# Optimization experiments

Hardware: AMD Instinct MI355X
Metric: run time of the kernel (lower is better)

Reference implementation:

```python
import jax, jax.numpy as jnp
import numpy as np


def setup_inputs() -> dict:
    key = jax.random.key(0)
    k1, k2, k3, k4 = jax.random.split(key, 4)
    B, Nq, Nk, D = 8, 2048, 2048, 768
    return {
        "query": jax.random.normal(k1, (B, Nq, D), dtype=jnp.float32),
        "key": jax.random.normal(k2, (Nk, D), dtype=jnp.float32),
        "x": jax.random.normal(k3, (B, Nk, D), dtype=jnp.float32),
        "W": jax.random.normal(k4, (D, D), dtype=jnp.float32) * (1.0 / np.sqrt(D)),
        "b": jnp.zeros((D,), dtype=jnp.float32),
    }


def reference(query, key, x, W, b):
    # Linear projection: [B,Nq,dk] @ W^T + b -> [B,Nq,dq]
    query_proj = jnp.einsum("bqd,ed->bqe", query, W) + b
    # tensordot over dim_query: [B,Nq,dq] x [Nk,dq] -> [B,Nq,Nk]
    score = jnp.einsum("bqe,ke->bqk", query_proj, key)
    attn = jax.nn.softmax(score, axis=-1)
    # bmm: [B,Nq,Nk] @ [B,Nk,Dv] -> [B,Nq,Dv]
    out = jnp.einsum("bqk,bkd->bqd", attn, x)
    return (out, attn)
```

## Files before the change

kernel.cpp:

```cpp
#include <hip/hip_runtime.h>

typedef short s16x8 __attribute__((ext_vector_type(8)));
typedef float f32x4 __attribute__((ext_vector_type(4)));

__device__ __forceinline__ unsigned short f2bf(float f) {
    unsigned int u = __builtin_bit_cast(unsigned int, f);
    u += 0x7FFFu + ((u >> 16) & 1u);
    return (unsigned short)(u >> 16);
}
__device__ __forceinline__ float bf2f(unsigned short h) {
    unsigned int u = ((unsigned int)h) << 16;
    return __builtin_bit_cast(float, u);
}

__device__ __forceinline__ int swz(int row, int kbyte) {
    return (row * 64 + kbyte) ^ (((row >> 1) & 3) << 4);
}

__device__ __forceinline__ void gl16(const void* g, void* l) {
    __builtin_amdgcn_global_load_lds(
        (__attribute__((address_space(1))) void*)(g),
        (__attribute__((address_space(3))) void*)(l), 16, 0, 0);
}

template<int SPLIT, bool TRANSB, bool BIAS>
__global__ __launch_bounds__(256, 1) void mfma_gemm(
    const float* __restrict__ A, const float* __restrict__ Bsrc,
    const float* __restrict__ bias, float* __restrict__ C,
    int M, int N, int K, long strideA, long strideB, long strideC)
{
    constexpr int NB = (SPLIT > 1) ? 2 : 1;
    __shared__ unsigned short sA[NB][128 * 32];
    __shared__ unsigned short sB[NB][128 * 32];

    const int t  = threadIdx.x;
    const int bz = blockIdx.z;
    const float* Ab = A    + (long)bz * strideA;
    const float* Bb = Bsrc + (long)bz * strideB;
    float*       Cb = C    + (long)bz * strideC;
    const int m0 = blockIdx.y * 128;
    const int n0 = blockIdx.x * 128;

    const int l  = t & 63, w = t >> 6;
    const int rm = (w >> 1) * 64;
    const int cn = (w & 1) * 64;
    const int lr = l & 15;
    const int kg = (l >> 4) * 16;

    const int srow = t >> 1;
    const int skh  = (t & 1) * 16;
    const int s_ = t & 15;
    const int kp = t >> 4;

    f32x4 acc[4][4];
    #pragma unroll
    for (int i = 0; i < 4; ++i)
        #pragma unroll
        for (int j = 0; j < 4; ++j)
            acc[i][j] = (f32x4){0.f, 0.f, 0.f, 0.f};

    for (int kt = 0; kt < K; kt += 32) {
        {
            const float* p = &Ab[(long)(m0 + srow) * K + kt + skh];
            float f[16];
            #pragma unroll
            for (int q = 0; q < 4; ++q) {
                const float4 v = *(const float4*)(p + 4 * q);
                f[4*q+0] = v.x; f[4*q+1] = v.y; f[4*q+2] = v.z; f[4*q+3] = v.w;
            }
            s16x8 h0, h1, l0, l1;
            #pragma unroll
            for (int q = 0; q < 8; ++q) {
                unsigned short h = f2bf(f[q]);      h0[q] = (short)h;
                if (SPLIT > 1) l0[q] = (short)f2bf(f[q] - bf2f(h));
                unsigned short g = f2bf(f[8 + q]);  h1[q] = (short)g;
                if (SPLIT > 1) l1[q] = (short)f2bf(f[8 + q] - bf2f(g));
            }
            *(s16x8*)((char*)sA[0] + swz(srow, skh * 2))      = h0;
            *(s16x8*)((char*)sA[0] + swz(srow, skh * 2 + 16)) = h1;
            if (SPLIT > 1) {
                *(s16x8*)((char*)sA[1] + swz(srow, skh * 2))      = l0;
                *(s16x8*)((char*)sA[1] + swz(srow, skh * 2 + 16)) = l1;
            }
        }
        if (!TRANSB) {
            const float* p = &Bb[(long)(n0 + srow) * K + kt + skh];
            float f[16];
            #pragma unroll
            for (int q = 0; q < 4; ++q) {
                const float4 v = *(const float4*)(p + 4 * q);
                f[4*q+0] = v.x; f[4*q+1] = v.y; f[4*q+2] = v.z; f[4*q+3] = v.w;
            }
            s16x8 h0, h1, l0, l1;
            #pragma unroll
            for (int q = 0; q < 8; ++q) {
                unsigned short h = f2bf(f[q]);      h0[q] = (short)h;
                if (SPLIT > 1) l0[q] = (short)f2bf(f[q] - bf2f(h));
                unsigned short g = f2bf(f[8 + q]);  h1[q] = (short)g;
                if (SPLIT > 1) l1[q] = (short)f2bf(f[8 + q] - bf2f(g));
            }
            *(s16x8*)((char*)sB[0] + swz(srow, skh * 2))      = h0;
            *(s16x8*)((char*)sB[0] + swz(srow, skh * 2 + 16)) = h1;
            if (SPLIT > 1) {
                *(s16x8*)((char*)sB[1] + swz(srow, skh * 2))      = l0;
                *(s16x8*)((char*)sB[1] + swz(srow, skh * 2 + 16)) = l1;
            }
        } else {
            const float* r0 = &Bb[(long)(kt + 2 * kp) * N + n0 + s_ * 8];
            const float* r1 = r0 + N;
            float a0[8], a1[8];
            {
                const float4 u0 = *(const float4*)(r0);
                const float4 u1 = *(const float4*)(r0 + 4);
                const float4 v0 = *(const float4*)(r1);
                const float4 v1 = *(const float4*)(r1 + 4);
                a0[0]=u0.x;a0[1]=u0.y;a0[2]=u0.z;a0[3]=u0.w;
                a0[4]=u1.x;a0[5]=u1.y;a0[6]=u1.z;a0[7]=u1.w;
                a1[0]=v0.x;a1[1]=v0.y;a1[2]=v0.z;a1[3]=v0.w;
                a1[4]=v1.x;a1[5]=v1.y;a1[6]=v1.z;a1[7]=v1.w;
            }
            #pragma unroll
            for (int j = 0; j < 8; ++j) {
                const int i  = (j + s_) & 7;
                const int nl = s_ * 8 + i;
                const unsigned int val =
                    (unsigned int)f2bf(a0[i]) | ((unsigned int)f2bf(a1[i]) << 16);
                *(unsigned int*)((char*)sB[0] + swz(nl, 4 * kp)) = val;
            }
        }
        __syncthreads();

        s16x8 ah[4], bh[4];
        #pragma unroll
        for (int mi = 0; mi < 4; ++mi)
            ah[mi] = *(const s16x8*)((const char*)sA[0] + swz(rm + mi * 16 + lr, kg));
        #pragma unroll
        for (int nj = 0; nj < 4; ++nj)
            bh[nj] = *(const s16x8*)((const char*)sB[0] + swz(cn + nj * 16 + lr, kg));
        #pragma unroll
        for (int mi = 0; mi < 4; ++mi)
            #pragma unroll
            for (int nj = 0; nj < 4; ++nj)
                acc[mi][nj] = __builtin_amdgcn_mfma_f32_16x16x32_bf16(
                    ah[mi], bh[nj], acc[mi][nj], 0, 0, 0);
        if (SPLIT > 1) {
            s16x8 al[4], bl[4];
            #pragma unroll
            for (int mi = 0; mi < 4; ++mi)
                al[mi] = *(const s16x8*)((const char*)sA[1] + swz(rm + mi * 16 + lr, kg));
            #pragma unroll
            for (int mi = 0; mi < 4; ++mi)
                #pragma unroll
                for (int nj = 0; nj < 4; ++nj)
                    acc[mi][nj] = __builtin_amdgcn_mfma_f32_16x16x32_bf16(
                        al[mi], bh[nj], acc[mi][nj], 0, 0, 0);
            #pragma unroll
            for (int nj = 0; nj < 4; ++nj)
                bl[nj] = *(const s16x8*)((const char*)sB[1] + swz(cn + nj * 16 + lr, kg));
            #pragma unroll
            for (int mi = 0; mi < 4; ++mi)
                #pragma unroll
                for (int nj = 0; nj < 4; ++nj)
                    acc[mi][nj] = __builtin_amdgcn_mfma_f32_16x16x32_bf16(
                        ah[mi], bl[nj], acc[mi][nj], 0, 0, 0);
        }
        __syncthreads();
    }

    #pragma unroll
    for (int mi = 0; mi < 4; ++mi) {
        #pragma unroll
        for (int nj = 0; nj < 4; ++nj) {
            const int row = m0 + rm + mi * 16 + (l >> 4) * 4;
            const int col = n0 + cn + nj * 16 + lr;
            const float badd = BIAS ? bias[col] : 0.f;
            #pragma unroll
            for (int r = 0; r < 4; ++r)
                Cb[(long)(row + r) * N + col] = acc[mi][nj][r] + badd;
        }
    }
}

__global__ __launch_bounds__(256, 1) void score_gemm(
    const unsigned short* __restrict__ Ah, const unsigned short* __restrict__ Al,
    const unsigned short* __restrict__ Bh, const unsigned short* __restrict__ Bl,
    const float* __restrict__ bias, float* __restrict__ C,
    int M, int N, int K, int nbx)
{
    __shared__ unsigned short sAh[128 * 32];
    __shared__ unsigned short sBh[128 * 32];
    __shared__ unsigned short sAl[128 * 32];
    __shared__ unsigned short sBl[128 * 32];

    const int bid = blockIdx.x;
    const int cpx = gridDim.x >> 3;
    const int sw  = (bid & 7) * cpx + (bid >> 3);
    const int mb  = sw / nbx, nb = sw % nbx;
    const int m0 = mb * 128, n0 = nb * 128;

    const int t = threadIdx.x;
    const int l = t & 63, w = t >> 6;
    const int rm = (w >> 1) * 64;
    const int cn = (w & 1) * 64;
    const int lr = l & 15;
    const int kg = (l >> 4) * 16;

    const int r0 = 2 * w, r1 = 2 * w + 1;
    const int rowS0 = 16 * r0 + (l >> 2);
    const int rowS1 = 16 * r1 + (l >> 2);
    const int h0 = (l & 3) ^ ((rowS0 >> 1) & 3);
    const int h1 = (l & 3) ^ ((rowS1 >> 1) & 3);

    const unsigned short* gAh0 = Ah + (long)(m0 + rowS0) * K + 8 * h0;
    const unsigned short* gAh1 = Ah + (long)(m0 + rowS1) * K + 8 * h1;
    const unsigned short* gAl0 = Al + (long)(m0 + rowS0) * K + 8 * h0;
    const unsigned short* gAl1 = Al + (long)(m0 + rowS1) * K + 8 * h1;
    const unsigned short* gBh0 = Bh + (long)(n0 + rowS0) * K + 8 * h0;
    const unsigned short* gBh1 = Bh + (long)(n0 + rowS1) * K + 8 * h1;
    const unsigned short* gBl0 = Bl + (long)(n0 + rowS0) * K + 8 * h0;
    const unsigned short* gBl1 = Bl + (long)(n0 + rowS1) * K + 8 * h1;

    unsigned short* dA0 = &sAh[r0 * 512];
    unsigned short* dA1 = &sAh[r1 * 512];
    unsigned short* dAl0 = &sAl[r0 * 512];
    unsigned short* dAl1 = &sAl[r1 * 512];
    unsigned short* dB0 = &sBh[r0 * 512];
    unsigned short* dB1 = &sBh[r1 * 512];
    unsigned short* dBl0 = &sBl[r0 * 512];
    unsigned short* dBl1 = &sBl[r1 * 512];

    f32x4 acc[4][4];
    #pragma unroll
    for (int i = 0; i < 4; ++i)
        #pragma unroll
        for (int j = 0; j < 4; ++j)
            acc[i][j] = (f32x4){0.f, 0.f, 0.f, 0.f};

    const int nk = K >> 5;
    for (int it = 0; it < nk; ++it) {
        gl16(gAh0, dA0);  gl16(gAh1, dA1);
        gl16(gBh0, dB0);  gl16(gBh1, dB1);
        gl16(gAl0, dAl0); gl16(gAl1, dAl1);
        gl16(gBl0, dBl0); gl16(gBl1, dBl1);
        gAh0 += 32; gAh1 += 32; gAl0 += 32; gAl1 += 32;
        gBh0 += 32; gBh1 += 32; gBl0 += 32; gBl1 += 32;
        __syncthreads();

        s16x8 ah[4], bh[4];
        #pragma unroll
        for (int mi = 0; mi < 4; ++mi)
            ah[mi] = *(const s16x8*)((const char*)sAh + swz(rm + mi * 16 + lr, kg));
        #pragma unroll
        for (int nj = 0; nj < 4; ++nj)
            bh[nj] = *(const s16x8*)((const char*)sBh + swz(cn + nj * 16 + lr, kg));
        #pragma unroll
        for (int mi = 0; mi < 4; ++mi)
            #pragma unroll
            for (int nj = 0; nj < 4; ++nj)
                acc[mi][nj] = __builtin_amdgcn_mfma_f32_16x16x32_bf16(
                    ah[mi], bh[nj], acc[mi][nj], 0, 0, 0);
        s16x8 al[4], bl[4];
        #pragma unroll
        for (int mi = 0; mi < 4; ++mi)
            al[mi] = *(const s16x8*)((const char*)sAl + swz(rm + mi * 16 + lr, kg));
        #pragma unroll
        for (int mi = 0; mi < 4; ++mi)
            #pragma unroll
            for (int nj = 0; nj < 4; ++nj)
                acc[mi][nj] = __builtin_amdgcn_mfma_f32_16x16x32_bf16(
                    al[mi], bh[nj], acc[mi][nj], 0, 0, 0);
        #pragma unroll
        for (int nj = 0; nj < 4; ++nj)
            bl[nj] = *(const s16x8*)((const char*)sBl + swz(cn + nj * 16 + lr, kg));
        #pragma unroll
        for (int mi = 0; mi < 4; ++mi)
            #pragma unroll
            for (int nj = 0; nj < 4; ++nj)
                acc[mi][nj] = __builtin_amdgcn_mfma_f32_16x16x32_bf16(
                    ah[mi], bl[nj], acc[mi][nj], 0, 0, 0);
        __syncthreads();
    }

    #pragma unroll
    for (int mi = 0; mi < 4; ++mi) {
        #pragma unroll
        for (int nj = 0; nj < 4; ++nj) {
            const int row = m0 + rm + mi * 16 + (l >> 4) * 4;
            const int col = n0 + cn + nj * 16 + lr;
            const float badd = bias[col];
            #pragma unroll
            for (int r = 0; r < 4; ++r)
                C[(long)(row + r) * N + col] = acc[mi][nj][r] + badd;
        }
    }
}

__global__ __launch_bounds__(256, 1) void out_gemm2(
    const unsigned short* __restrict__ A16, const unsigned short* __restrict__ B16,
    float* __restrict__ C, int M, int N, int K,
    long strideA, long strideB, long strideC)
{
    __shared__ unsigned short sA[128 * 32];
    __shared__ unsigned short sB[128 * 32];

    const int bz = blockIdx.z;
    const unsigned short* Ab = A16 + (long)bz * strideA;
    const unsigned short* Bb = B16 + (long)bz * strideB;
    float* Cb = C + (long)bz * strideC;
    const int m0 = blockIdx.x * 128;
    const int n0 = blockIdx.y * 128;

    const int t = threadIdx.x;
    const int l = t & 63, w = t >> 6;
    const int rm = (w >> 1) * 64;
    const int cn = (w & 1) * 64;
    const int lr = l & 15;
    const int kg = (l >> 4) * 16;

    const int r0 = 2 * w, r1 = 2 * w + 1;
    const int rowS0 = 16 * r0 + (l >> 2);
    const int rowS1 = 16 * r1 + (l >> 2);
    const int h0 = (l & 3) ^ ((rowS0 >> 1) & 3);
    const int h1 = (l & 3) ^ ((rowS1 >> 1) & 3);

    const unsigned short* gA0 = Ab + (long)(m0 + rowS0) * K + 8 * h0;
    const unsigned short* gA1 = Ab + (long)(m0 + rowS1) * K + 8 * h1;
    const unsigned short* gB0 = Bb + (long)(n0 + rowS0) * K + 8 * h0;
    const unsigned short* gB1 = Bb + (long)(n0 + rowS1) * K + 8 * h1;
    unsigned short* dA0 = &sA[r0 * 512];
    unsigned short* dA1 = &sA[r1 * 512];
    unsigned short* dB0 = &sB[r0 * 512];
    unsigned short* dB1 = &sB[r1 * 512];

    f32x4 acc[4][4];
    #pragma unroll
    for (int i = 0; i < 4; ++i)
        #pragma unroll
        for (int j = 0; j < 4; ++j)
            acc[i][j] = (f32x4){0.f, 0.f, 0.f, 0.f};

    const int nk = K >> 5;
    for (int it = 0; it < nk; ++it) {
        gl16(gA0, dA0); gl16(gA1, dA1);
        gl16(gB0, dB0); gl16(gB1, dB1);
        gA0 += 32; gA1 += 32; gB0 += 32; gB1 += 32;
        __syncthreads();

        s16x8 ah[4], bh[4];
        #pragma unroll
        for (int mi = 0; mi < 4; ++mi)
            ah[mi] = *(const s16x8*)((const char*)sA + swz(rm + mi * 16 + lr, kg));
        #pragma unroll
        for (int nj = 0; nj < 4; ++nj)
            bh[nj] = *(const s16x8*)((const char*)sB + swz(cn + nj * 16 + lr, kg));
        #pragma unroll
        for (int mi = 0; mi < 4; ++mi)
            #pragma unroll
            for (int nj = 0; nj < 4; ++nj)
                acc[mi][nj] = __builtin_amdgcn_mfma_f32_16x16x32_bf16(
                    ah[mi], bh[nj], acc[mi][nj], 0, 0, 0);
        __syncthreads();
    }

    #pragma unroll
    for (int mi = 0; mi < 4; ++mi) {
        #pragma unroll
        for (int nj = 0; nj < 4; ++nj) {
            const int row = m0 + rm + mi * 16 + (l >> 4) * 4;
            const int col = n0 + cn + nj * 16 + lr;
            #pragma unroll
            for (int r = 0; r < 4; ++r)
                Cb[(long)(row + r) * N + col] = acc[mi][nj][r];
        }
    }
}

__global__ __launch_bounds__(256, 1) void out_gemm(
    const float* __restrict__ A32, const unsigned short* __restrict__ B16,
    float* __restrict__ C, int M, int N, int K,
    long strideA, long strideB, long strideC)
{
    __shared__ unsigned short sA[128 * 32];
    __shared__ unsigned short sB[128 * 32];

    const int bz = blockIdx.z;
    const float* Ab = A32 + (long)bz * strideA;
    const unsigned short* Bb = B16 + (long)bz * strideB;
    float* Cb = C + (long)bz * strideC;
    const int m0 = blockIdx.x * 128;
    const int n0 = blockIdx.y * 128;

    const int t = threadIdx.x;
    const int l = t & 63, w = t >> 6;
    const int rm = (w >> 1) * 64;
    const int cn = (w & 1) * 64;
    const int lr = l & 15;
    const int kg = (l >> 4) * 16;

    const int r0 = 2 * w, r1 = 2 * w + 1;
    const int rowS0 = 16 * r0 + (l >> 2);
    const int rowS1 = 16 * r1 + (l >> 2);
    const int h0 = (l & 3) ^ ((rowS0 >> 1) & 3);
    const int h1 = (l & 3) ^ ((rowS1 >> 1) & 3);
    const unsigned short* gB0 = Bb + (long)(n0 + rowS0) * K + 8 * h0;
    const unsigned short* gB1 = Bb + (long)(n0 + rowS1) * K + 8 * h1;
    unsigned short* dB0 = &sB[r0 * 512];
    unsigned short* dB1 = &sB[r1 * 512];

    const int srow = t >> 1;
    const int skh  = (t & 1) * 16;
    const float* gA = &Ab[(long)(m0 + srow) * K + skh];

    f32x4 acc[4][4];
    #pragma unroll
    for (int i = 0; i < 4; ++i)
        #pragma unroll
        for (int j = 0; j < 4; ++j)
            acc[i][j] = (f32x4){0.f, 0.f, 0.f, 0.f};

    const int nk = K >> 5;
    for (int it = 0; it < nk; ++it) {
        gl16(gB0, dB0); gl16(gB1, dB1);
        gB0 += 32; gB1 += 32;
        {
            float f[16];
            #pragma unroll
            for (int q = 0; q < 4; ++q) {
                const float4 v = *(const float4*)(gA + 4 * q);
                f[4*q+0] = v.x; f[4*q+1] = v.y; f[4*q+2] = v.z; f[4*q+3] = v.w;
            }
            gA += 32;
            s16x8 v0, v1;
            #pragma unroll
            for (int q = 0; q < 8; ++q) {
                v0[q] = (short)f2bf(f[q]);
                v1[q] = (short)f2bf(f[8 + q]);
            }
            *(s16x8*)((char*)sA + swz(srow, skh * 2))      = v0;
            *(s16x8*)((char*)sA + swz(srow, skh * 2 + 16)) = v1;
        }
        __syncthreads();

        s16x8 ah[4], bh[4];
        #pragma unroll
        for (int mi = 0; mi < 4; ++mi)
            ah[mi] = *(const s16x8*)((const char*)sA + swz(rm + mi * 16 + lr, kg));
        #pragma unroll
        for (int nj = 0; nj < 4; ++nj)
            bh[nj] = *(const s16x8*)((const char*)sB + swz(cn + nj * 16 + lr, kg));
        #pragma unroll
        for (int mi = 0; mi < 4; ++mi)
            #pragma unroll
            for (int nj = 0; nj < 4; ++nj)
                acc[mi][nj] = __builtin_amdgcn_mfma_f32_16x16x32_bf16(
                    ah[mi], bh[nj], acc[mi][nj], 0, 0, 0);
        __syncthreads();
    }

    #pragma unroll
    for (int mi = 0; mi < 4; ++mi) {
        #pragma unroll
        for (int nj = 0; nj < 4; ++nj) {
            const int row = m0 + rm + mi * 16 + (l >> 4) * 4;
            const int col = n0 + cn + nj * 16 + lr;
            #pragma unroll
            for (int r = 0; r < 4; ++r)
                Cb[(long)(row + r) * N + col] = acc[mi][nj][r];
        }
    }
}

template<bool TOBF16>
__global__ __launch_bounds__(256) void transpose64(
    const float* __restrict__ in, void* __restrict__ outv,
    int R, int Cc, long sIn, long sOut)
{
    __shared__ float tl[64][65];
    const int z = blockIdx.z;
    const float* ib = in + (long)z * sIn;
    const int r0 = blockIdx.x * 64, c0 = blockIdx.y * 64;
    const int t = threadIdx.x;
    const int lrr = t >> 4, lc = (t & 15) * 4;
    #pragma unroll
    for (int p = 0; p < 4; ++p) {
        const float4 v = *(const float4*)&ib[(long)(r0 + lrr + 16 * p) * Cc + c0 + lc];
        tl[lrr + 16 * p][lc + 0] = v.x; tl[lrr + 16 * p][lc + 1] = v.y;
        tl[lrr + 16 * p][lc + 2] = v.z; tl[lrr + 16 * p][lc + 3] = v.w;
    }
    __syncthreads();
    #pragma unroll
    for (int p = 0; p < 4; ++p) {
        const int orow = c0 + lrr + 16 * p;
        const int ocol = r0 + lc;
        const float a = tl[lc + 0][lrr + 16 * p];
        const float b = tl[lc + 1][lrr + 16 * p];
        const float c = tl[lc + 2][lrr + 16 * p];
        const float d = tl[lc + 3][lrr + 16 * p];
        if (TOBF16) {
            ushort4 u = { f2bf(a), f2bf(b), f2bf(c), f2bf(d) };
            *(ushort4*)((unsigned short*)outv + (long)z * sOut + (long)orow * R + ocol) = u;
        } else {
            float4 u = { a, b, c, d };
            *(float4*)((float*)outv + (long)z * sOut + (long)orow * R + ocol) = u;
        }
    }
}

__global__ __launch_bounds__(256) void convert_hilo(
    const float* __restrict__ src, unsigned short* __restrict__ hi,
    unsigned short* __restrict__ lo, long n8)
{
    for (long i = (long)blockIdx.x * blockDim.x + threadIdx.x; i < n8;
         i += (long)gridDim.x * blockDim.x) {
        const float4 a = *(const float4*)&src[i * 8];
        const float4 b = *(const float4*)&src[i * 8 + 4];
        const float f[8] = { a.x, a.y, a.z, a.w, b.x, b.y, b.z, b.w };
        s16x8 h, lv;
        #pragma unroll
        for (int q = 0; q < 8; ++q) {
            const unsigned short hh = f2bf(f[q]);
            h[q]  = (short)hh;
            lv[q] = (short)f2bf(f[q] - bf2f(hh));
        }
        *(s16x8*)&hi[i * 8] = h;
        *(s16x8*)&lo[i * 8] = lv;
    }
}

__global__ __launch_bounds__(256) void bk_dot(
    const float* __restrict__ key, const float* __restrict__ b,
    float* __restrict__ bk, int D)
{
    const int row = blockIdx.x * 4 + (threadIdx.x >> 6);
    const int l = threadIdx.x & 63;
    const float* kr = key + (long)row * D;
    float s = 0.f;
    for (int e = l; e < D; e += 64) s += kr[e] * b[e];
    #pragma unroll
    for (int off = 32; off > 0; off >>= 1) s += __shfl_xor(s, off);
    if (l == 0) bk[row] = s;
}

__global__ __launch_bounds__(256) void softmax_bf16(
    float* __restrict__ S, unsigned short* __restrict__ S16, int cols)
{
    const long row = blockIdx.x;
    float* p = S + row * (long)cols;
    unsigned short* p16 = S16 + row * (long)cols;
    const int t = threadIdx.x;
    const int wid = t >> 6;
    const int base = t * 8;

    const float4 a = *(const float4*)&p[base];
    const float4 b = *(const float4*)&p[base + 4];
    float vals[8] = { a.x, a.y, a.z, a.w, b.x, b.y, b.z, b.w };
    float m = -INFINITY;
    #pragma unroll
    for (int i = 0; i < 8; ++i) m = fmaxf(m, vals[i]);
    #pragma unroll
    for (int off = 32; off > 0; off >>= 1)
        m = fmaxf(m, __shfl_xor(m, off));
    __shared__ float smax[4], ssum[4];
    if ((t & 63) == 0) smax[wid] = m;
    __syncthreads();
    m = fmaxf(fmaxf(smax[0], smax[1]), fmaxf(smax[2], smax[3]));

    float s = 0.f;
    #pragma unroll
    for (int i = 0; i < 8; ++i) {
        vals[i] = __expf(vals[i] - m);
        s += vals[i];
    }
    #pragma unroll
    for (int off = 32; off > 0; off >>= 1)
        s += __shfl_xor(s, off);
    if ((t & 63) == 0) ssum[wid] = s;
    __syncthreads();
    s = (ssum[0] + ssum[1]) + (ssum[2] + ssum[3]);
    const float inv = 1.0f / s;

    float4 o0, o1;
    o0.x = vals[0]*inv; o0.y = vals[1]*inv; o0.z = vals[2]*inv; o0.w = vals[3]*inv;
    o1.x = vals[4]*inv; o1.y = vals[5]*inv; o1.z = vals[6]*inv; o1.w = vals[7]*inv;
    *(float4*)&p[base]     = o0;
    *(float4*)&p[base + 4] = o1;
    s16x8 h;
    h[0]=(short)f2bf(o0.x); h[1]=(short)f2bf(o0.y); h[2]=(short)f2bf(o0.z); h[3]=(short)f2bf(o0.w);
    h[4]=(short)f2bf(o1.x); h[5]=(short)f2bf(o1.y); h[6]=(short)f2bf(o1.z); h[7]=(short)f2bf(o1.w);
    *(s16x8*)&p16[base] = h;
}

__global__ __launch_bounds__(256) void softmax_rows(float* __restrict__ S, int cols)
{
    const long row = blockIdx.x;
    float* p = S + row * (long)cols;
    const int t = threadIdx.x;
    const int wid = t >> 6;

    float vals[8];
    float m = -INFINITY;
    #pragma unroll
    for (int i = 0; i < 8; ++i) {
        vals[i] = p[t + i * 256];
        m = fmaxf(m, vals[i]);
    }
    #pragma unroll
    for (int off = 32; off > 0; off >>= 1)
        m = fmaxf(m, __shfl_xor(m, off));
    __shared__ float smax[4], ssum[4];
    if ((t & 63) == 0) smax[wid] = m;
    __syncthreads();
    m = fmaxf(fmaxf(smax[0], smax[1]), fmaxf(smax[2], smax[3]));

    float s = 0.f;
    #pragma unroll
    for (int i = 0; i < 8; ++i) {
        vals[i] = __expf(vals[i] - m);
        s += vals[i];
    }
    #pragma unroll
    for (int off = 32; off > 0; off >>= 1)
        s += __shfl_xor(s, off);
    if ((t & 63) == 0) ssum[wid] = s;
    __syncthreads();
    s = (ssum[0] + ssum[1]) + (ssum[2] + ssum[3]);
    const float inv = 1.0f / s;
    #pragma unroll
    for (int i = 0; i < 8; ++i)
        p[t + i * 256] = vals[i] * inv;
}

extern "C" void kernel_launch(void* const* d_in, const int* in_sizes, int n_in,
                              void* d_out, int out_size, void* d_ws, size_t ws_size,
                              hipStream_t stream)
{
    const float* query = (const float*)d_in[0];
    const float* key   = (const float*)d_in[1];
    const float* x     = (const float*)d_in[2];
    const float* W     = (const float*)d_in[3];
    const float* bias  = (const float*)d_in[4];

    const int D  = in_sizes[4];
    const int Nk = in_sizes[1] / D;
    const int B  = in_sizes[2] / (Nk * D);
    const int Nq = in_sizes[0] / (B * D);

    float* out  = (float*)d_out;
    float* attn = out + (long)B * Nq * D;

    const long nQ  = (long)B * Nq * D;
    const long nKW = (long)Nk * D;
    const long nX  = (long)B * Nk * D;

    const size_t xTb   = (size_t)nX * 2;
    const size_t qLob  = (size_t)nQ * 2;
    const size_t atb1  = (size_t)Nq * Nk * 2;
    const size_t wsMin = xTb + qLob;

    int g = 0;
    if (ws_size >= wsMin) {
        size_t avail = ws_size - xTb;
        if (avail < qLob) avail = 0;
        g = (int)((ws_size - xTb) / atb1);
        if (g > B) g = B;
    }

    if (g >= 2) {
        unsigned short* q_hi  = (unsigned short*)out;
        unsigned short* KW_hi = q_hi + nQ;
        unsigned short* KW_lo = KW_hi + nKW;
        float*          bk    = (float*)(KW_lo + nKW);
        unsigned short* xT     = (unsigned short*)d_ws;
        unsigned short* q_lo   = (unsigned short*)((char*)d_ws + xTb);
        unsigned short* attn16 = (unsigned short*)((char*)d_ws + xTb);
        float* Wt  = attn;
        float* KWf = attn + 1048576;

        dim3 gtw(D / 64, D / 64, 1);
        transpose64<false><<<gtw, 256, 0, stream>>>(W, Wt, D, D, 0L, 0L);
        dim3 gkw(D / 128, Nk / 128, 1);
        mfma_gemm<3, false, false><<<gkw, 256, 0, stream>>>(
            key, Wt, nullptr, KWf, Nk, D, D, 0L, 0L, 0L);
        convert_hilo<<<768, 256, 0, stream>>>(KWf, KW_hi, KW_lo, nKW / 8);
        bk_dot<<<Nk / 4, 256, 0, stream>>>(key, bias, bk, D);
        convert_hilo<<<2048, 256, 0, stream>>>(query, q_hi, q_lo, nQ / 8);
        dim3 gtx(Nk / 64, D / 64, B);
        transpose64<true><<<gtx, 256, 0, stream>>>(
            x, xT, Nk, D, (long)Nk * D, (long)D * Nk);
        const int nbx = Nk / 128;
        const int nwg = (B * Nq / 128) * nbx;
        score_gemm<<<nwg, 256, 0, stream>>>(
            q_hi, q_lo, KW_hi, KW_lo, bk, attn, B * Nq, Nk, D, nbx);

        for (int b0 = 0; b0 < B; b0 += g) {
            const int gb = (b0 + g <= B) ? g : (B - b0);
            softmax_bf16<<<gb * Nq, 256, 0, stream>>>(
                attn + (long)b0 * Nq * Nk, attn16, Nk);
            dim3 go(Nq / 128, D / 128, gb);
            out_gemm2<<<go, 256, 0, stream>>>(
                attn16, xT + (long)b0 * D * Nk, out + (long)b0 * Nq * D,
                Nq, D, Nk, (long)Nq * Nk, (long)D * Nk, (long)Nq * D);
        }
    } else if (ws_size >= wsMin) {
        unsigned short* q_hi  = (unsigned short*)out;
        unsigned short* KW_hi = q_hi + nQ;
        unsigned short* KW_lo = KW_hi + nKW;
        float*          bk    = (float*)(KW_lo + nKW);
        unsigned short* q_lo  = (unsigned short*)d_ws;
        unsigned short* xT    = q_lo + nQ;
        float* Wt  = attn;
        float* KWf = attn + 1048576;

        dim3 gtw(D / 64, D / 64, 1);
        transpose64<false><<<gtw, 256, 0, stream>>>(W, Wt, D, D, 0L, 0L);
        dim3 gkw(D / 128, Nk / 128, 1);
        mfma_gemm<3, false, false><<<gkw, 256, 0, stream>>>(
            key, Wt, nullptr, KWf, Nk, D, D, 0L, 0L, 0L);
        convert_hilo<<<768, 256, 0, stream>>>(KWf, KW_hi, KW_lo, nKW / 8);
        bk_dot<<<Nk / 4, 256, 0, stream>>>(key, bias, bk, D);
        convert_hilo<<<2048, 256, 0, stream>>>(query, q_hi, q_lo, nQ / 8);
        dim3 gtx(Nk / 64, D / 64, B);
        transpose64<true><<<gtx, 256, 0, stream>>>(
            x, xT, Nk, D, (long)Nk * D, (long)D * Nk);
        const int nbx = Nk / 128;
        const int nwg = (B * Nq / 128) * nbx;
        score_gemm<<<nwg, 256, 0, stream>>>(
            q_hi, q_lo, KW_hi, KW_lo, bk, attn, B * Nq, Nk, D, nbx);
        softmax_rows<<<B * Nq, 256, 0, stream>>>(attn, Nk);
        dim3 go(Nq / 128, D / 128, B);
        out_gemm<<<go, 256, 0, stream>>>(
            attn, xT, out, Nq, D, Nk, (long)Nq * Nk, (long)D * Nk, (long)Nq * D);
    } else {
        float* qp = out;
        dim3 g1(D / 128, (B * Nq) / 128, 1);
        mfma_gemm<3, false, true><<<g1, 256, 0, stream>>>(
            query, W, bias, qp, B * Nq, D, D, 0L, 0L, 0L);
        dim3 g2(Nk / 128, Nq / 128, B);
        mfma_gemm<3, false, false><<<g2, 256, 0, stream>>>(
            qp, key, nullptr, attn, Nq, Nk, D, (long)Nq * D, 0L, (long)Nq * Nk);
        softmax_rows<<<B * Nq, 256, 0, stream>>>(attn, Nk);
        dim3 g4(D / 128, Nq / 128, B);
        mfma_gemm<1, true, false><<<g4, 256, 0, stream>>>(
            attn, x, nullptr, out, Nq, D, Nk, (long)Nq * Nk, (long)Nk * D, (long)Nq * D);
    }
}
```

Measured before the change: 381.5 us.

## Switch score and output GEMMs from bf16 to fp16 and drop key low part

Converts the split-precision score GEMM from bf16 hi/lo to fp16 hi/lo. Because fp16 carries more mantissa bits, the key-side low term (ah*bl) is dropped, cutting a third of the MFMAs and a quarter of the LDS traffic per K step. Softmax output and the transposed x are also stored as fp16, and the output GEMM uses fp16 MFMA. The trade-off is fp16's narrower exponent range, which could overflow or lose accuracy for large score or query values.

```diff
diff --git a/kernel.cpp b/kernel.cpp
--- a/kernel.cpp
+++ b/kernel.cpp
@@ -1,6 +1,7 @@
 #include <hip/hip_runtime.h>
 
 typedef short s16x8 __attribute__((ext_vector_type(8)));
+typedef _Float16 h16x8 __attribute__((ext_vector_type(8)));
 typedef float f32x4 __attribute__((ext_vector_type(4)));
 
 __device__ __forceinline__ unsigned short f2bf(float f) {
@@ -11,6 +12,13 @@
 __device__ __forceinline__ float bf2f(unsigned short h) {
     unsigned int u = ((unsigned int)h) << 16;
     return __builtin_bit_cast(float, u);
+}
+__device__ __forceinline__ unsigned short f2h(float f) {
+    _Float16 h = (_Float16)f;
+    return __builtin_bit_cast(unsigned short, h);
+}
+__device__ __forceinline__ float h2f(unsigned short u) {
+    return (float)__builtin_bit_cast(_Float16, u);
 }
 
 __device__ __forceinline__ int swz(int row, int kbyte) {
@@ -181,16 +189,15 @@
     }
 }
 
-__global__ __launch_bounds__(256, 1) void score_gemm(
+__global__ __launch_bounds__(256, 1) void score_gemm_f16(
     const unsigned short* __restrict__ Ah, const unsigned short* __restrict__ Al,
-    const unsigned short* __restrict__ Bh, const unsigned short* __restrict__ Bl,
+    const unsigned short* __restrict__ Bh,
     const float* __restrict__ bias, float* __restrict__ C,
     int M, int N, int K, int nbx)
 {
     __shared__ unsigned short sAh[128 * 32];
+    __shared__ unsigned short sAl[128 * 32];
     __shared__ unsigned short sBh[128 * 32];
-    __shared__ unsigned short sAl[128 * 32];
-    __shared__ unsigned short sBl[128 * 32];
 
     const int bid = blockIdx.x;
     const int cpx = gridDim.x >> 3;
@@ -217,17 +224,13 @@
     const unsigned short* gAl1 = Al + (long)(m0 + rowS1) * K + 8 * h1;
     const unsigned short* gBh0 = Bh + (long)(n0 + rowS0) * K + 8 * h0;
     const unsigned short* gBh1 = Bh + (long)(n0 + rowS1) * K + 8 * h1;
-    const unsigned short* gBl0 = Bl + (long)(n0 + rowS0) * K + 8 * h0;
-    const unsigned short* gBl1 = Bl + (long)(n0 + rowS1) * K + 8 * h1;
-
-    unsigned short* dA0 = &sAh[r0 * 512];
-    unsigned short* dA1 = &sAh[r1 * 512];
+
+    unsigned short* dA0  = &sAh[r0 * 512];
+    unsigned short* dA1  = &sAh[r1 * 512];
     unsigned short* dAl0 = &sAl[r0 * 512];
     unsigned short* dAl1 = &sAl[r1 * 512];
-    unsigned short* dB0 = &sBh[r0 * 512];
-    unsigned short* dB1 = &sBh[r1 * 512];
-    unsigned short* dBl0 = &sBl[r0 * 512];
-    unsigned short* dBl1 = &sBl[r1 * 512];
+    unsigned short* dB0  = &sBh[r0 * 512];
+    unsigned short* dB1  = &sBh[r1 * 512];
 
     f32x4 acc[4][4];
     #pragma unroll
@@ -241,43 +244,36 @@
         gl16(gAh0, dA0);  gl16(gAh1, dA1);
         gl16(gBh0, dB0);  gl16(gBh1, dB1);
         gl16(gAl0, dAl0); gl16(gAl1, dAl1);
-        gl16(gBl0, dBl0); gl16(gBl1, dBl1);
         gAh0 += 32; gAh1 += 32; gAl0 += 32; gAl1 += 32;
-        gBh0 += 32; gBh1 += 32; gBl0 += 32; gBl1 += 32;
-        __syncthreads();
-
-        s16x8 ah[4], bh[4];
-        #pragma unroll
-        for (int mi = 0; mi < 4; ++mi)
-            ah[mi] = *(const s16x8*)((const char*)sAh + swz(rm + mi * 16 + lr, kg));
+        gBh0 += 32; gBh1 += 32;
+        __syncthreads();
+
+        h16x8 ah[4], bh[4];
+        #pragma unroll
+        for (int mi = 0; mi < 4; ++mi)
+            ah[mi] = __builtin_bit_cast(h16x8,
+                *(const s16x8*)((const char*)sAh + swz(rm + mi * 16 + lr, kg)));
         #pragma unroll
         for (int nj = 0; nj < 4; ++nj)
-            bh[nj] = *(const s16x8*)((const char*)sBh + swz(cn + nj * 16 + lr, kg));
+            bh[nj] = __builtin_bit_cast(h16x8,
+                *(const s16x8*)((const char*)sBh + swz(cn + nj * 16 + lr, kg)));
         #pragma unroll
         for (int mi = 0; mi < 4; ++mi)
             #pragma unroll
             for (int nj = 0; nj < 4; ++nj)
-                acc[mi][nj] = __builtin_amdgcn_mfma_f32_16x16x32_bf16(
+                acc[mi][nj] = __builtin_amdgcn_mfma_f32_16x16x32_f16(
                     ah[mi], bh[nj], acc[mi][nj], 0, 0, 0);
-        s16x8 al[4], bl[4];
-        #pragma unroll
-        for (int mi = 0; mi < 4; ++mi)
-            al[mi] = *(const s16x8*)((const char*)sAl + swz(rm + mi * 16 + lr, kg));
+        h16x8 al[4];
+        #pragma unroll
+        for (int mi = 0; mi < 4; ++mi)
+            al[mi] = __builtin_bit_cast(h16x8,
+                *(const s16x8*)((const char*)sAl + swz(rm + mi * 16 + lr, kg)));
         #pragma unroll
         for (int mi = 0; mi < 4; ++mi)
             #pragma unroll
             for (int nj = 0; nj < 4; ++nj)
-                acc[mi][nj] = __builtin_amdgcn_mfma_f32_16x16x32_bf16(
+                acc[mi][nj] = __builtin_amdgcn_mfma_f32_16x16x32_f16(
                     al[mi], bh[nj], acc[mi][nj], 0, 0, 0);
-        #pragma unroll
-        for (int nj = 0; nj < 4; ++nj)
-            bl[nj] = *(const s16x8*)((const char*)sBl + swz(cn + nj * 16 + lr, kg));
-        #pragma unroll
-        for (int mi = 0; mi < 4; ++mi)
-            #pragma unroll
-            for (int nj = 0; nj < 4; ++nj)
-                acc[mi][nj] = __builtin_amdgcn_mfma_f32_16x16x32_bf16(
-                    ah[mi], bl[nj], acc[mi][nj], 0, 0, 0);
         __syncthreads();
     }
 
@@ -295,7 +291,7 @@
     }
 }
 
-__global__ __launch_bounds__(256, 1) void out_gemm2(
+__global__ __launch_bounds__(256, 1) void out_gemm3(
     const unsigned short* __restrict__ A16, const unsigned short* __restrict__ B16,
     float* __restrict__ C, int M, int N, int K,
     long strideA, long strideB, long strideC)
@@ -346,18 +342,20 @@
         gA0 += 32; gA1 += 32; gB0 += 32; gB1 += 32;
         __syncthreads();
 
-        s16x8 ah[4], bh[4];
-        #pragma unroll
-        for (int mi = 0; mi < 4; ++mi)
-            ah[mi] = *(const s16x8*)((const char*)sA + swz(rm + mi * 16 + lr, kg));
+        h16x8 ah[4], bh[4];
+        #pragma unroll
+        for (int mi = 0; mi < 4; ++mi)
+            ah[mi] = __builtin_bit_cast(h16x8,
+                *(const s16x8*)((const char*)sA + swz(rm + mi * 16 + lr, kg)));
         #pragma unroll
         for (int nj = 0; nj < 4; ++nj)
-            bh[nj] = *(const s16x8*)((const char*)sB + swz(cn + nj * 16 + lr, kg));
+            bh[nj] = __builtin_bit_cast(h16x8,
+                *(const s16x8*)((const char*)sB + swz(cn + nj * 16 + lr, kg)));
         #pragma unroll
         for (int mi = 0; mi < 4; ++mi)
             #pragma unroll
             for (int nj = 0; nj < 4; ++nj)
-                acc[mi][nj] = __builtin_amdgcn_mfma_f32_16x16x32_bf16(
+                acc[mi][nj] = __builtin_amdgcn_mfma_f32_16x16x32_f16(
                     ah[mi], bh[nj], acc[mi][nj], 0, 0, 0);
         __syncthreads();
     }
@@ -470,7 +468,121 @@
     }
 }
 
-template<bool TOBF16>
+__global__ __launch_bounds__(256, 1) void score_gemm(
+    const unsigned short* __restrict__ Ah, const unsigned short* __restrict__ Al,
+    const unsigned short* __restrict__ Bh, const unsigned short* __restrict__ Bl,
+    const float* __restrict__ bias, float* __restrict__ C,
+    int M, int N, int K, int nbx)
+{
+    __shared__ unsigned short sAh[128 * 32];
+    __shared__ unsigned short sBh[128 * 32];
+    __shared__ unsigned short sAl[128 * 32];
+    __shared__ unsigned short sBl[128 * 32];
+
+    const int bid = blockIdx.x;
+    const int cpx = gridDim.x >> 3;
+    const int sw  = (bid & 7) * cpx + (bid >> 3);
+    const int mb  = sw / nbx, nb = sw % nbx;
+    const int m0 = mb * 128, n0 = nb * 128;
+
+    const int t = threadIdx.x;
+    const int l = t & 63, w = t >> 6;
+    const int rm = (w >> 1) * 64;
+    const int cn = (w & 1) * 64;
+    const int lr = l & 15;
+    const int kg = (l >> 4) * 16;
+
+    const int r0 = 2 * w, r1 = 2 * w + 1;
+    const int rowS0 = 16 * r0 + (l >> 2);
+    const int rowS1 = 16 * r1 + (l >> 2);
+    const int h0 = (l & 3) ^ ((rowS0 >> 1) & 3);
+    const int h1 = (l & 3) ^ ((rowS1 >> 1) & 3);
+
+    const unsigned short* gAh0 = Ah + (long)(m0 + rowS0) * K + 8 * h0;
+    const unsigned short* gAh1 = Ah + (long)(m0 + rowS1) * K + 8 * h1;
+    const unsigned short* gAl0 = Al + (long)(m0 + rowS0) * K + 8 * h0;
+    const unsigned short* gAl1 = Al + (long)(m0 + rowS1) * K + 8 * h1;
+    const unsigned short* gBh0 = Bh + (long)(n0 + rowS0) * K + 8 * h0;
+    const unsigned short* gBh1 = Bh + (long)(n0 + rowS1) * K + 8 * h1;
+    const unsigned short* gBl0 = Bl + (long)(n0 + rowS0) * K + 8 * h0;
+    const unsigned short* gBl1 = Bl + (long)(n0 + rowS1) * K + 8 * h1;
+
+    unsigned short* dA0 = &sAh[r0 * 512];
+    unsigned short* dA1 = &sAh[r1 * 512];
+    unsigned short* dAl0 = &sAl[r0 * 512];
+    unsigned short* dAl1 = &sAl[r1 * 512];
+    unsigned short* dB0 = &sBh[r0 * 512];
+    unsigned short* dB1 = &sBh[r1 * 512];
+    unsigned short* dBl0 = &sBl[r0 * 512];
+    unsigned short* dBl1 = &sBl[r1 * 512];
+
+    f32x4 acc[4][4];
+    #pragma unroll
+    for (int i = 0; i < 4; ++i)
+        #pragma unroll
+        for (int j = 0; j < 4; ++j)
+            acc[i][j] = (f32x4){0.f, 0.f, 0.f, 0.f};
+
+    const int nk = K >> 5;
+    for (int it = 0; it < nk; ++it) {
+        gl16(gAh0, dA0);  gl16(gAh1, dA1);
+        gl16(gBh0, dB0);  gl16(gBh1, dB1);
+        gl16(gAl0, dAl0); gl16(gAl1, dAl1);
+        gl16(gBl0, dBl0); gl16(gBl1, dBl1);
+        gAh0 += 32; gAh1 += 32; gAl0 += 32; gAl1 += 32;
+        gBh0 += 32; gBh1 += 32; gBl0 += 32; gBl1 += 32;
+        __syncthreads();
+
+        s16x8 ah[4], bh[4];
+        #pragma unroll
+        for (int mi = 0; mi < 4; ++mi)
+            ah[mi] = *(const s16x8*)((const char*)sAh + swz(rm + mi * 16 + lr, kg));
+        #pragma unroll
+        for (int nj = 0; nj < 4; ++nj)
+            bh[nj] = *(const s16x8*)((const char*)sBh + swz(cn + nj * 16 + lr, kg));
+        #pragma unroll
+        for (int mi = 0; mi < 4; ++mi)
+            #pragma unroll
+            for (int nj = 0; nj < 4; ++nj)
+                acc[mi][nj] = __builtin_amdgcn_mfma_f32_16x16x32_bf16(
+                    ah[mi], bh[nj], acc[mi][nj], 0, 0, 0);
+        s16x8 al[4], bl[4];
+        #pragma unroll
+        for (int mi = 0; mi < 4; ++mi)
+            al[mi] = *(const s16x8*)((const char*)sAl + swz(rm + mi * 16 + lr, kg));
+        #pragma unroll
+        for (int mi = 0; mi < 4; ++mi)
+            #pragma unroll
+            for (int nj = 0; nj < 4; ++nj)
+                acc[mi][nj] = __builtin_amdgcn_mfma_f32_16x16x32_bf16(
+                    al[mi], bh[nj], acc[mi][nj], 0, 0, 0);
+        #pragma unroll
+        for (int nj = 0; nj < 4; ++nj)
+            bl[nj] = *(const s16x8*)((const char*)sBl + swz(cn + nj * 16 + lr, kg));
+        #pragma unroll
+        for (int mi = 0; mi < 4; ++mi)
+            #pragma unroll
+            for (int nj = 0; nj < 4; ++nj)
+                acc[mi][nj] = __builtin_amdgcn_mfma_f32_16x16x32_bf16(
+                    ah[mi], bl[nj], acc[mi][nj], 0, 0, 0);
+        __syncthreads();
+    }
+
+    #pragma unroll
+    for (int mi = 0; mi < 4; ++mi) {
+        #pragma unroll
+        for (int nj = 0; nj < 4; ++nj) {
+            const int row = m0 + rm + mi * 16 + (l >> 4) * 4;
+            const int col = n0 + cn + nj * 16 + lr;
+            const float badd = bias[col];
+            #pragma unroll
+            for (int r = 0; r < 4; ++r)
+                C[(long)(row + r) * N + col] = acc[mi][nj][r] + badd;
+        }
+    }
+}
+
+template<int MODE>
 __global__ __launch_bounds__(256) void transpose64(
     const float* __restrict__ in, void* __restrict__ outv,
     int R, int Cc, long sIn, long sOut)
@@ -496,8 +608,11 @@
         const float b = tl[lc + 1][lrr + 16 * p];
         const float c = tl[lc + 2][lrr + 16 * p];
         const float d = tl[lc + 3][lrr + 16 * p];
-        if (TOBF16) {
+        if (MODE == 1) {
             ushort4 u = { f2bf(a), f2bf(b), f2bf(c), f2bf(d) };
+            *(ushort4*)((unsigned short*)outv + (long)z * sOut + (long)orow * R + ocol) = u;
+        } else if (MODE == 2) {
+            ushort4 u = { f2h(a), f2h(b), f2h(c), f2h(d) };
             *(ushort4*)((unsigned short*)outv + (long)z * sOut + (long)orow * R + ocol) = u;
         } else {
             float4 u = { a, b, c, d };
@@ -527,6 +642,27 @@
     }
 }
 
+__global__ __launch_bounds__(256) void convert_hilo_f16(
+    const float* __restrict__ src, unsigned short* __restrict__ hi,
+    unsigned short* __restrict__ lo, long n8)
+{
+    for (long i = (long)blockIdx.x * blockDim.x + threadIdx.x; i < n8;
+         i += (long)gridDim.x * blockDim.x) {
+        const float4 a = *(const float4*)&src[i * 8];
+        const float4 b = *(const float4*)&src[i * 8 + 4];
+        const float f[8] = { a.x, a.y, a.z, a.w, b.x, b.y, b.z, b.w };
+        s16x8 h, lv;
+        #pragma unroll
+        for (int q = 0; q < 8; ++q) {
+            const unsigned short hh = f2h(f[q]);
+            h[q]  = (short)hh;
+            lv[q] = (short)f2h(f[q] - h2f(hh));
+        }
+        *(s16x8*)&hi[i * 8] = h;
+        *(s16x8*)&lo[i * 8] = lv;
+    }
+}
+
 __global__ __launch_bounds__(256) void bk_dot(
     const float* __restrict__ key, const float* __restrict__ b,
     float* __restrict__ bk, int D)
@@ -541,7 +677,7 @@
     if (l == 0) bk[row] = s;
 }
 
-__global__ __launch_bounds__(256) void softmax_bf16(
+__global__ __launch_bounds__(256) void softmax_f16(
     float* __restrict__ S, unsigned short* __restrict__ S16, int cols)
 {
     const long row = blockIdx.x;
@@ -585,8 +721,8 @@
     *(float4*)&p[base]     = o0;
     *(float4*)&p[base + 4] = o1;
     s16x8 h;
-    h[0]=(short)f2bf(o0.x); h[1]=(short)f2bf(o0.y); h[2]=(short)f2bf(o0.z); h[3]=(short)f2bf(o0.w);
-    h[4]=(short)f2bf(o1.x); h[5]=(short)f2bf(o1.y); h[6]=(short)f2bf(o1.z); h[7]=(short)f2bf(o1.w);
+    h[0]=(short)f2h(o0.x); h[1]=(short)f2h(o0.y); h[2]=(short)f2h(o0.z); h[3]=(short)f2h(o0.w);
+    h[4]=(short)f2h(o1.x); h[5]=(short)f2h(o1.y); h[6]=(short)f2h(o1.z); h[7]=(short)f2h(o1.w);
     *(s16x8*)&p16[base] = h;
 }
 
@@ -659,8 +795,6 @@
 
     int g = 0;
     if (ws_size >= wsMin) {
-        size_t avail = ws_size - xTb;
-        if (avail < qLob) avail = 0;
         g = (int)((ws_size - xTb) / atb1);
         if (g > B) g = B;
     }
@@ -677,27 +811,27 @@
         float* KWf = attn + 1048576;
 
         dim3 gtw(D / 64, D / 64, 1);
-        transpose64<false><<<gtw, 256, 0, stream>>>(W, Wt, D, D, 0L, 0L);
+        transpose64<0><<<gtw, 256, 0, stream>>>(W, Wt, D, D, 0L, 0L);
         dim3 gkw(D / 128, Nk / 128, 1);
         mfma_gemm<3, false, false><<<gkw, 256, 0, stream>>>(
             key, Wt, nullptr, KWf, Nk, D, D, 0L, 0L, 0L);
-        convert_hilo<<<768, 256, 0, stream>>>(KWf, KW_hi, KW_lo, nKW / 8);
+        convert_hilo_f16<<<768, 256, 0, stream>>>(KWf, KW_hi, KW_lo, nKW / 8);
         bk_dot<<<Nk / 4, 256, 0, stream>>>(key, bias, bk, D);
-        convert_hilo<<<2048, 256, 0, stream>>>(query, q_hi, q_lo, nQ / 8);
+        convert_hilo_f16<<<2048, 256, 0, stream>>>(query, q_hi, q_lo, nQ / 8);
         dim3 gtx(Nk / 64, D / 64, B);
-        transpose64<true><<<gtx, 256, 0, stream>>>(
+        transpose64<2><<<gtx, 256, 0, stream>>>(
             x, xT, Nk, D, (long)Nk * D, (long)D * Nk);
         const int nbx = Nk / 128;
         const int nwg = (B * Nq / 128) * nbx;
-        score_gemm<<<nwg, 256, 0, stream>>>(
-            q_hi, q_lo, KW_hi, KW_lo, bk, attn, B * Nq, Nk, D, nbx);
+        score_gemm_f16<<<nwg, 256, 0, stream>>>(
+            q_hi, q_lo, KW_hi, bk, attn, B * Nq, Nk, D, nbx);
 
         for (int b0 = 0; b0 < B; b0 += g) {
             const int gb = (b0 + g <= B) ? g : (B - b0);
-            softmax_bf16<<<gb * Nq, 256, 0, stream>>>(
+            softmax_f16<<<gb * Nq, 256, 0, stream>>>(
                 attn + (long)b0 * Nq * Nk, attn16, Nk);
             dim3 go(Nq / 128, D / 128, gb);
-            out_gemm2<<<go, 256, 0, stream>>>(
+            out_gemm3<<<go, 256, 0, stream>>>(
                 attn16, xT + (long)b0 * D * Nk, out + (long)b0 * Nq * D,
                 Nq, D, Nk, (long)Nq * Nk, (long)D * Nk, (long)Nq * D);
         }
@@ -712,7 +846,7 @@
         float* KWf = attn + 1048576;
 
         dim3 gtw(D / 64, D / 64, 1);
-        transpose64<false><<<gtw, 256, 0, stream>>>(W, Wt, D, D, 0L, 0L);
+        transpose64<0><<<gtw, 256, 0, stream>>>(W, Wt, D, D, 0L, 0L);
         dim3 gkw(D / 128, Nk / 128, 1);
         mfma_gemm<3, false, false><<<gkw, 256, 0, stream>>>(
             key, Wt, nullptr, KWf, Nk, D, D, 0L, 0L, 0L);
@@ -720,7 +854,7 @@
         bk_dot<<<Nk / 4, 256, 0, stream>>>(key, bias, bk, D);
         convert_hilo<<<2048, 256, 0, stream>>>(query, q_hi, q_lo, nQ / 8);
         dim3 gtx(Nk / 64, D / 64, B);
-        transpose64<true><<<gtx, 256, 0, stream>>>(
+        transpose64<1><<<gtx, 256, 0, stream>>>(
             x, xT, Nk, D, (long)Nk * D, (long)D * Nk);
         const int nbx = Nk / 128;
         const int nwg = (B * Nq / 128) * nbx;
```

New measurement: 352.4 us. 7.6% less time.
